# Kernel tuning notes

Hardware: AMD Instinct MI355X
Metric: run time of the kernel (lower is better)

Reference implementation:

```python
import jax, jax.numpy as jnp
import numpy as np

N = 8192  # num_nodes
E = 8192  # num_edges (== N so self-loops sit on the diagonal)
C = 256   # in_channels
ALPHA = 0.1
BETA = 0.5


def setup_inputs() -> dict:
    key = jax.random.key(0)
    k1, k2, k3 = jax.random.split(key, 3)
    x_0 = jax.random.normal(k1, (N, C), dtype=jnp.float32)
    # binary hypergraph incidence with self-loops on the diagonal
    mask = (jax.random.uniform(k2, (N, E)) < 0.004).astype(jnp.float32)
    idx = jnp.arange(N)
    incidence_1 = mask.at[idx, idx].set(1.0)
    # torch Linear(C, C, bias=False) weight, Kaiming-uniform-ish scale
    W = jax.random.normal(k3, (C, C), dtype=jnp.float32) / jnp.sqrt(C)
    return {"x_0": x_0, "incidence_1": incidence_1, "W": W}


def reference(x_0, incidence_1, W):
    # 1) edge aggregation: m_{0->1} = B^T x  -> [E, C]
    m_0_1 = incidence_1.T @ x_0
    # degree normalization (matches diag/to_dense math without materializing diag)
    node_degree = jnp.sum(incidence_1, axis=1)                      # [N]
    edge_degree = (node_degree @ incidence_1) / jnp.sum(incidence_1, axis=0)  # [E]
    # 2) node aggregation with 1/sqrt(d_z), 1/sqrt(d_x) scaling
    m_1_0 = (incidence_1 @ (m_0_1 / jnp.sqrt(edge_degree)[:, None])) \
            / jnp.sqrt(node_degree)[:, None]                        # [N, C]
    # 3) skip + learned update (x_skip defaults to x_0)
    x_combined = (1.0 - ALPHA) * m_1_0 + ALPHA * x_0
    return (1.0 - BETA) * x_combined + BETA * (x_combined @ W.T)
```

## Files before the change

### kernel.cpp

```cpp
#include <hip/hip_runtime.h>
#include <hip/hip_bf16.h>

#define NN 8192
#define NE 8192
#define CC 256
#define CAP 128

typedef __attribute__((ext_vector_type(8))) short bf16x8;
typedef __attribute__((ext_vector_type(8))) unsigned short u16x8;
typedef __attribute__((ext_vector_type(4))) float f32x4;

static __device__ __forceinline__ ushort f2b(float f) {
    unsigned u = __float_as_uint(f);
    return (ushort)((u + 0x7fffu + ((u >> 16) & 1u)) >> 16);
}
static __device__ __forceinline__ float b2f(ushort u) {
    return __uint_as_float((unsigned)u << 16);
}

__global__ __launch_bounds__(256) void k1_scan(const float* __restrict__ B,
                                               const float* __restrict__ x0,
                                               const float* __restrict__ W,
                                               ushort* __restrict__ x0b,
                                               ushort* __restrict__ Wb,
                                               int* __restrict__ csr,
                                               int* __restrict__ row_cnt,
                                               int* __restrict__ col_cnt,
                                               int* __restrict__ csc,
                                               float* __restrict__ edge_wsum) {
    {
        int i = blockIdx.x * 1024 + threadIdx.x * 4;
        float4 v = *(const float4*)(x0 + i);
        ushort4 u; u.x = f2b(v.x); u.y = f2b(v.y); u.z = f2b(v.z); u.w = f2b(v.w);
        *(ushort4*)(x0b + i) = u;
        if (blockIdx.x < 64) {
            float4 w = *(const float4*)(W + i);
            ushort4 uw; uw.x = f2b(w.x); uw.y = f2b(w.y); uw.z = f2b(w.z); uw.w = f2b(w.w);
            *(ushort4*)(Wb + i) = uw;
        }
    }
    const int wave = threadIdx.x >> 6;
    const int lane = threadIdx.x & 63;
    const int row  = blockIdx.x * 4 + wave;
    const float4* rp = (const float4*)(B + (size_t)row * NE);
    int* outp = csr + (size_t)row * CAP;
    const unsigned long long mlt = (1ull << lane) - 1ull;
    int base = 0;
    for (int it = 0; it < NE / 256; ++it) {
        float4 v = rp[it * 64 + lane];
        unsigned long long bx = __ballot(v.x != 0.f);
        unsigned long long by = __ballot(v.y != 0.f);
        unsigned long long bz = __ballot(v.z != 0.f);
        unsigned long long bw = __ballot(v.w != 0.f);
        if (!(bx | by | bz | bw)) continue;
        int tx = __popcll(bx), ty = __popcll(by), tz = __popcll(bz), tw = __popcll(bw);
        int e0 = (it * 64 + lane) * 4;
        int p;
        if (v.x != 0.f) { p = base + __popcll(bx & mlt);                if (p < CAP) outp[p] = e0;     }
        if (v.y != 0.f) { p = base + tx + __popcll(by & mlt);           if (p < CAP) outp[p] = e0 + 1; }
        if (v.z != 0.f) { p = base + tx + ty + __popcll(bz & mlt);      if (p < CAP) outp[p] = e0 + 2; }
        if (v.w != 0.f) { p = base + tx + ty + tz + __popcll(bw & mlt); if (p < CAP) outp[p] = e0 + 3; }
        base += tx + ty + tz + tw;
    }
    const int cnt = base < CAP ? base : CAP;
    if (lane == 0) row_cnt[row] = cnt;
    const float deg = (float)cnt;
    for (int i = lane; i < cnt; i += 64) {
        int e = outp[i];
        int pos = atomicAdd(&col_cnt[e], 1);
        if (pos < CAP) csc[(size_t)e * CAP + pos] = row;
        atomicAdd(&edge_wsum[e], deg);
    }
}

__global__ __launch_bounds__(256) void k4_edge_agg(const ushort* __restrict__ x0b,
                                                   const int* __restrict__ csc,
                                                   const int* __restrict__ col_cnt,
                                                   const float* __restrict__ edge_wsum,
                                                   ushort* __restrict__ m01s) {
    const int wave = threadIdx.x >> 6;
    const int lane = threadIdx.x & 63;
    const int half = lane >> 5;
    const int cl = lane & 31;
    const int e = blockIdx.x * 4 + wave;
    int cnt = col_cnt[e]; if (cnt > CAP) cnt = CAP;
    const float er = rsqrtf(edge_wsum[e] / (float)cnt);
    const int* cp = csc + (size_t)e * CAP;
    const int idx = cp[lane];
    const ushort* xb = x0b + cl * 8;
    float a0[8] = {}, a1[8] = {};
    const int lim = cnt < 64 ? cnt : 64;
    int i = 0;
    for (; i + 4 <= lim; i += 4) {
        int na = __shfl(idx, i + half);
        int nb = __shfl(idx, i + 2 + half);
        u16x8 a = *(const u16x8*)(xb + (size_t)na * CC);
        u16x8 b = *(const u16x8*)(xb + (size_t)nb * CC);
        #pragma unroll
        for (int c = 0; c < 8; ++c) { a0[c] += b2f(a[c]); a1[c] += b2f(b[c]); }
    }
    if (i + 2 <= lim) {
        int na = __shfl(idx, i + half);
        u16x8 a = *(const u16x8*)(xb + (size_t)na * CC);
        #pragma unroll
        for (int c = 0; c < 8; ++c) a0[c] += b2f(a[c]);
        i += 2;
    }
    if (i < lim) {
        int na = __shfl(idx, i);
        if (half == 0) {
            u16x8 a = *(const u16x8*)(xb + (size_t)na * CC);
            #pragma unroll
            for (int c = 0; c < 8; ++c) a0[c] += b2f(a[c]);
        }
    }
    if (cnt > 64 && half == 0) {
        for (int j = 64; j < cnt; ++j) {
            int n2 = cp[j];
            u16x8 a = *(const u16x8*)(xb + (size_t)n2 * CC);
            #pragma unroll
            for (int c = 0; c < 8; ++c) a0[c] += b2f(a[c]);
        }
    }
    u16x8 r8;
    #pragma unroll
    for (int c = 0; c < 8; ++c) {
        float t = a0[c] + a1[c];
        t += __shfl_xor(t, 32);
        r8[c] = f2b(t * er);
    }
    if (half == 0) *(u16x8*)(m01s + (size_t)e * CC + cl * 8) = r8;
}

__global__ __launch_bounds__(1024, 8) void k5_fused(const ushort* __restrict__ x0b,
                                                    const ushort* __restrict__ m01s,
                                                    const int* __restrict__ csr,
                                                    const int* __restrict__ row_cnt,
                                                    const ushort* __restrict__ Wb,
                                                    float* __restrict__ out) {
    __shared__ __align__(16) ushort xs[16][264];
    const int w = threadIdx.x >> 6;
    const int lane = threadIdx.x & 63;
    const int half = lane >> 5;
    const int cl = lane & 31;
    const int n = blockIdx.x * 16 + w;
    const int cnt = row_cnt[n];
    const float nr = rsqrtf((float)cnt);
    const int* ep = csr + (size_t)n * CAP;
    const int idx = ep[lane];
    const ushort* mb = m01s + cl * 8;
    float a0[8] = {}, a1[8] = {};
    const int lim = cnt < 64 ? cnt : 64;
    int i = 0;
    for (; i + 4 <= lim; i += 4) {
        int ea = __shfl(idx, i + half);
        int eb = __shfl(idx, i + 2 + half);
        u16x8 a = *(const u16x8*)(mb + (size_t)ea * CC);
        u16x8 b = *(const u16x8*)(mb + (size_t)eb * CC);
        #pragma unroll
        for (int c = 0; c < 8; ++c) { a0[c] += b2f(a[c]); a1[c] += b2f(b[c]); }
    }
    if (i + 2 <= lim) {
        int ea = __shfl(idx, i + half);
        u16x8 a = *(const u16x8*)(mb + (size_t)ea * CC);
        #pragma unroll
        for (int c = 0; c < 8; ++c) a0[c] += b2f(a[c]);
        i += 2;
    }
    if (i < lim) {
        int ea = __shfl(idx, i);
        if (half == 0) {
            u16x8 a = *(const u16x8*)(mb + (size_t)ea * CC);
            #pragma unroll
            for (int c = 0; c < 8; ++c) a0[c] += b2f(a[c]);
        }
    }
    if (cnt > 64 && half == 0) {
        for (int j = 64; j < cnt; ++j) {
            int e2 = ep[j];
            u16x8 a = *(const u16x8*)(mb + (size_t)e2 * CC);
            #pragma unroll
            for (int c = 0; c < 8; ++c) a0[c] += b2f(a[c]);
        }
    }
    u16x8 x = *(const u16x8*)(x0b + (size_t)n * CC + cl * 8);
    const float s = 0.9f * nr;
    u16x8 r8;
    #pragma unroll
    for (int c = 0; c < 8; ++c) {
        float t = a0[c] + a1[c];
        t += __shfl_xor(t, 32);
        r8[c] = f2b(s * t + 0.1f * b2f(x[c]));
    }
    if (half == 0) *(u16x8*)(&xs[w][cl * 8]) = r8;
    __syncthreads();
    const int lr = lane & 15, lk = lane >> 4;
    const int n0 = w * 16;
    f32x4 acc = {0.f, 0.f, 0.f, 0.f};
    #pragma unroll
    for (int kb = 0; kb < 8; ++kb) {
        bf16x8 a = *(const bf16x8*)(&xs[lr][kb * 32 + lk * 8]);
        bf16x8 b = *(const bf16x8*)(Wb + (size_t)(n0 + lr) * CC + kb * 32 + lk * 8);
        acc = __builtin_amdgcn_mfma_f32_16x16x32_bf16(a, b, acc, 0, 0, 0);
    }
    const size_t rb = (size_t)blockIdx.x * 16;
    #pragma unroll
    for (int r = 0; r < 4; ++r) {
        int row = lk * 4 + r;
        int col = n0 + lr;
        float sk = b2f(xs[row][col]);
        out[(rb + row) * CC + col] = 0.5f * sk + 0.5f * acc[r];
    }
}

extern "C" void kernel_launch(void* const* d_in, const int* in_sizes, int n_in,
                              void* d_out, int out_size, void* d_ws, size_t ws_size,
                              hipStream_t stream) {
    const float* x0 = (const float*)d_in[0];
    const float* B  = (const float*)d_in[1];
    const float* W  = (const float*)d_in[2];
    float* out = (float*)d_out;

    char* ws = (char*)d_ws;
    const size_t need = (17ull << 20) + 4ull * NE * 4;
    if (ws_size < need) return;

    int*    csr       = (int*)(ws);
    int*    csc       = (int*)(ws + (4ull << 20));
    ushort* m01s      = (ushort*)(ws + (8ull << 20));
    ushort* x0b       = (ushort*)(ws + (12ull << 20));
    ushort* Wb        = (ushort*)(ws + (16ull << 20));
    int*    row_cnt   = (int*)(ws + (16ull << 20) + (256u << 10));
    int*    col_cnt   = row_cnt + NN;
    float*  edge_wsum = (float*)(col_cnt + NE);

    hipMemsetAsync(col_cnt, 0, 2ull * NE * 4, stream);

    k1_scan<<<NN / 4, 256, 0, stream>>>(B, x0, W, x0b, Wb, csr, row_cnt, col_cnt, csc, edge_wsum);
    k4_edge_agg<<<NE / 4, 256, 0, stream>>>(x0b, csc, col_cnt, edge_wsum, m01s);
    k5_fused<<<NN / 16, 1024, 0, stream>>>(x0b, m01s, csr, row_cnt, Wb, out);
}
```

Before: 104.7 us.

## Prefetch incidence rows in scan and deepen gather unrolling in aggregation kernels

The incidence-row scan now loads the next float4 before processing the current one. It replaces the four-ballot prefix compaction with a per-wave LDS atomic counter that hands each lane a slot range sized by the sum of its four values. The edge and node aggregation kernels now keep four gathered rows in flight per iteration instead of two, to raise memory-level parallelism. The LDS atomic makes the order of CSR entries nondeterministic. Using the value sum as the nonzero count assumes the incidence is strictly binary.

Measured after the change: 103.8 us. Within noise of the previous version (-0.8%).

```diff
diff --git a/kernel.cpp b/kernel.cpp
--- a/kernel.cpp
+++ b/kernel.cpp
@@ -28,6 +28,7 @@
                                                int* __restrict__ col_cnt,
                                                int* __restrict__ csc,
                                                float* __restrict__ edge_wsum) {
+    __shared__ int wcnt[4];
     {
         int i = blockIdx.x * 1024 + threadIdx.x * 4;
         float4 v = *(const float4*)(x0 + i);
@@ -44,25 +45,27 @@
     const int row  = blockIdx.x * 4 + wave;
     const float4* rp = (const float4*)(B + (size_t)row * NE);
     int* outp = csr + (size_t)row * CAP;
-    const unsigned long long mlt = (1ull << lane) - 1ull;
-    int base = 0;
-    for (int it = 0; it < NE / 256; ++it) {
-        float4 v = rp[it * 64 + lane];
-        unsigned long long bx = __ballot(v.x != 0.f);
-        unsigned long long by = __ballot(v.y != 0.f);
-        unsigned long long bz = __ballot(v.z != 0.f);
-        unsigned long long bw = __ballot(v.w != 0.f);
-        if (!(bx | by | bz | bw)) continue;
-        int tx = __popcll(bx), ty = __popcll(by), tz = __popcll(bz), tw = __popcll(bw);
-        int e0 = (it * 64 + lane) * 4;
-        int p;
-        if (v.x != 0.f) { p = base + __popcll(bx & mlt);                if (p < CAP) outp[p] = e0;     }
-        if (v.y != 0.f) { p = base + tx + __popcll(by & mlt);           if (p < CAP) outp[p] = e0 + 1; }
-        if (v.z != 0.f) { p = base + tx + ty + __popcll(bz & mlt);      if (p < CAP) outp[p] = e0 + 2; }
-        if (v.w != 0.f) { p = base + tx + ty + tz + __popcll(bw & mlt); if (p < CAP) outp[p] = e0 + 3; }
-        base += tx + ty + tz + tw;
-    }
-    const int cnt = base < CAP ? base : CAP;
+    if (lane == 0) wcnt[wave] = 0;
+    float4 v = rp[lane];
+    #pragma unroll 1
+    for (int it = 0; it < 32; ++it) {
+        float4 vn = v;
+        if (it < 31) vn = rp[(it + 1) * 64 + lane];
+        float fs = v.x + v.y + v.z + v.w;
+        if (__ballot(fs != 0.f)) {
+            int m = (int)fs;
+            int pos = 0;
+            if (m) pos = atomicAdd(&wcnt[wave], m);
+            int e0 = (it * 64 + lane) * 4;
+            if (v.x != 0.f) { if (pos < CAP) outp[pos] = e0;     ++pos; }
+            if (v.y != 0.f) { if (pos < CAP) outp[pos] = e0 + 1; ++pos; }
+            if (v.z != 0.f) { if (pos < CAP) outp[pos] = e0 + 2; ++pos; }
+            if (v.w != 0.f) { if (pos < CAP) outp[pos] = e0 + 3; ++pos; }
+        }
+        v = vn;
+    }
+    int cnt = wcnt[wave];
+    cnt = cnt < CAP ? cnt : CAP;
     if (lane == 0) row_cnt[row] = cnt;
     const float deg = (float)cnt;
     for (int i = lane; i < cnt; i += 64) {
@@ -91,35 +94,41 @@
     float a0[8] = {}, a1[8] = {};
     const int lim = cnt < 64 ? cnt : 64;
     int i = 0;
-    for (; i + 4 <= lim; i += 4) {
-        int na = __shfl(idx, i + half);
-        int nb = __shfl(idx, i + 2 + half);
-        u16x8 a = *(const u16x8*)(xb + (size_t)na * CC);
-        u16x8 b = *(const u16x8*)(xb + (size_t)nb * CC);
-        #pragma unroll
-        for (int c = 0; c < 8; ++c) { a0[c] += b2f(a[c]); a1[c] += b2f(b[c]); }
-    }
-    if (i + 2 <= lim) {
-        int na = __shfl(idx, i + half);
-        u16x8 a = *(const u16x8*)(xb + (size_t)na * CC);
-        #pragma unroll
-        for (int c = 0; c < 8; ++c) a0[c] += b2f(a[c]);
-        i += 2;
+    for (; i + 8 <= lim; i += 8) {
+        int n0 = __shfl(idx, i + half);
+        int n1 = __shfl(idx, i + 2 + half);
+        int n2 = __shfl(idx, i + 4 + half);
+        int n3 = __shfl(idx, i + 6 + half);
+        u16x8 r0 = *(const u16x8*)(xb + (size_t)n0 * CC);
+        u16x8 r1 = *(const u16x8*)(xb + (size_t)n1 * CC);
+        u16x8 r2 = *(const u16x8*)(xb + (size_t)n2 * CC);
+        u16x8 r3 = *(const u16x8*)(xb + (size_t)n3 * CC);
+        #pragma unroll
+        for (int c = 0; c < 8; ++c) {
+            a0[c] += b2f(r0[c]); a1[c] += b2f(r1[c]);
+            a0[c] += b2f(r2[c]); a1[c] += b2f(r3[c]);
+        }
+    }
+    for (; i + 2 <= lim; i += 2) {
+        int n0 = __shfl(idx, i + half);
+        u16x8 r0 = *(const u16x8*)(xb + (size_t)n0 * CC);
+        #pragma unroll
+        for (int c = 0; c < 8; ++c) a0[c] += b2f(r0[c]);
     }
     if (i < lim) {
-        int na = __shfl(idx, i);
+        int n0 = __shfl(idx, i);
         if (half == 0) {
-            u16x8 a = *(const u16x8*)(xb + (size_t)na * CC);
-            #pragma unroll
-            for (int c = 0; c < 8; ++c) a0[c] += b2f(a[c]);
+            u16x8 r0 = *(const u16x8*)(xb + (size_t)n0 * CC);
+            #pragma unroll
+            for (int c = 0; c < 8; ++c) a0[c] += b2f(r0[c]);
         }
     }
     if (cnt > 64 && half == 0) {
         for (int j = 64; j < cnt; ++j) {
             int n2 = cp[j];
-            u16x8 a = *(const u16x8*)(xb + (size_t)n2 * CC);
-            #pragma unroll
-            for (int c = 0; c < 8; ++c) a0[c] += b2f(a[c]);
+            u16x8 r0 = *(const u16x8*)(xb + (size_t)n2 * CC);
+            #pragma unroll
+            for (int c = 0; c < 8; ++c) a0[c] += b2f(r0[c]);
         }
     }
     u16x8 r8;
@@ -152,35 +161,41 @@
     float a0[8] = {}, a1[8] = {};
     const int lim = cnt < 64 ? cnt : 64;
     int i = 0;
-    for (; i + 4 <= lim; i += 4) {
-        int ea = __shfl(idx, i + half);
-        int eb = __shfl(idx, i + 2 + half);
-        u16x8 a = *(const u16x8*)(mb + (size_t)ea * CC);
-        u16x8 b = *(const u16x8*)(mb + (size_t)eb * CC);
-        #pragma unroll
-        for (int c = 0; c < 8; ++c) { a0[c] += b2f(a[c]); a1[c] += b2f(b[c]); }
-    }
-    if (i + 2 <= lim) {
-        int ea = __shfl(idx, i + half);
-        u16x8 a = *(const u16x8*)(mb + (size_t)ea * CC);
-        #pragma unroll
-        for (int c = 0; c < 8; ++c) a0[c] += b2f(a[c]);
-        i += 2;
+    for (; i + 8 <= lim; i += 8) {
+        int e0 = __shfl(idx, i + half);
+        int e1 = __shfl(idx, i + 2 + half);
+        int e2 = __shfl(idx, i + 4 + half);
+        int e3 = __shfl(idx, i + 6 + half);
+        u16x8 r0 = *(const u16x8*)(mb + (size_t)e0 * CC);
+        u16x8 r1 = *(const u16x8*)(mb + (size_t)e1 * CC);
+        u16x8 r2 = *(const u16x8*)(mb + (size_t)e2 * CC);
+        u16x8 r3 = *(const u16x8*)(mb + (size_t)e3 * CC);
+        #pragma unroll
+        for (int c = 0; c < 8; ++c) {
+            a0[c] += b2f(r0[c]); a1[c] += b2f(r1[c]);
+            a0[c] += b2f(r2[c]); a1[c] += b2f(r3[c]);
+        }
+    }
+    for (; i + 2 <= lim; i += 2) {
+        int e0 = __shfl(idx, i + half);
+        u16x8 r0 = *(const u16x8*)(mb + (size_t)e0 * CC);
+        #pragma unroll
+        for (int c = 0; c < 8; ++c) a0[c] += b2f(r0[c]);
     }
     if (i < lim) {
-        int ea = __shfl(idx, i);
+        int e0 = __shfl(idx, i);
         if (half == 0) {
-            u16x8 a = *(const u16x8*)(mb + (size_t)ea * CC);
-            #pragma unroll
-            for (int c = 0; c < 8; ++c) a0[c] += b2f(a[c]);
+            u16x8 r0 = *(const u16x8*)(mb + (size_t)e0 * CC);
+            #pragma unroll
+            for (int c = 0; c < 8; ++c) a0[c] += b2f(r0[c]);
         }
     }
     if (cnt > 64 && half == 0) {
         for (int j = 64; j < cnt; ++j) {
             int e2 = ep[j];
-            u16x8 a = *(const u16x8*)(mb + (size_t)e2 * CC);
-            #pragma unroll
-            for (int c = 0; c < 8; ++c) a0[c] += b2f(a[c]);
+            u16x8 r0 = *(const u16x8*)(mb + (size_t)e2 * CC);
+            #pragma unroll
+            for (int c = 0; c < 8; ++c) a0[c] += b2f(r0[c]);
         }
     }
     u16x8 x = *(const u16x8*)(x0b + (size_t)n * CC + cl * 8);
```

## Scan incidence by column panels and fuse edge aggregation into scan kernel

Applied to the files above, without the earlier changes.

Replaces the row-wise scan plus separate edge-aggregation kernel with a column-panel scan that builds CSC lists in shared memory and immediately gathers x0 rows for each edge. Edge-degree normalisation moves out of the edge pass into a small kernel and is applied per edge inside the node aggregation instead. CSR is built with global atomics per row, so neighbour order in each row is no longer deterministic, and x0 conversion moves to a separate kernel. The aim is to drop the memset and global CSC atomics, at the cost of one more launch and strided column-panel reads of the dense incidence matrix.

Result: slower. 147.3 us (+40.7%).

```diff
diff --git a/kernel.cpp b/kernel.cpp
--- a/kernel.cpp
+++ b/kernel.cpp
@@ -5,6 +5,7 @@
 #define NE 8192
 #define CC 256
 #define CAP 128
+#define PNL 32
 
 typedef __attribute__((ext_vector_type(8))) short bf16x8;
 typedef __attribute__((ext_vector_type(8))) unsigned short u16x8;
@@ -18,124 +19,137 @@
     return __uint_as_float((unsigned)u << 16);
 }
 
-__global__ __launch_bounds__(256) void k1_scan(const float* __restrict__ B,
-                                               const float* __restrict__ x0,
-                                               const float* __restrict__ W,
-                                               ushort* __restrict__ x0b,
-                                               ushort* __restrict__ Wb,
-                                               int* __restrict__ csr,
-                                               int* __restrict__ row_cnt,
-                                               int* __restrict__ col_cnt,
-                                               int* __restrict__ csc,
-                                               float* __restrict__ edge_wsum) {
-    {
-        int i = blockIdx.x * 1024 + threadIdx.x * 4;
-        float4 v = *(const float4*)(x0 + i);
-        ushort4 u; u.x = f2b(v.x); u.y = f2b(v.y); u.z = f2b(v.z); u.w = f2b(v.w);
-        *(ushort4*)(x0b + i) = u;
-        if (blockIdx.x < 64) {
-            float4 w = *(const float4*)(W + i);
-            ushort4 uw; uw.x = f2b(w.x); uw.y = f2b(w.y); uw.z = f2b(w.z); uw.w = f2b(w.w);
-            *(ushort4*)(Wb + i) = uw;
-        }
-    }
-    const int wave = threadIdx.x >> 6;
-    const int lane = threadIdx.x & 63;
-    const int row  = blockIdx.x * 4 + wave;
-    const float4* rp = (const float4*)(B + (size_t)row * NE);
-    int* outp = csr + (size_t)row * CAP;
-    const unsigned long long mlt = (1ull << lane) - 1ull;
-    int base = 0;
-    for (int it = 0; it < NE / 256; ++it) {
-        float4 v = rp[it * 64 + lane];
-        unsigned long long bx = __ballot(v.x != 0.f);
-        unsigned long long by = __ballot(v.y != 0.f);
-        unsigned long long bz = __ballot(v.z != 0.f);
-        unsigned long long bw = __ballot(v.w != 0.f);
-        if (!(bx | by | bz | bw)) continue;
-        int tx = __popcll(bx), ty = __popcll(by), tz = __popcll(bz), tw = __popcll(bw);
-        int e0 = (it * 64 + lane) * 4;
-        int p;
-        if (v.x != 0.f) { p = base + __popcll(bx & mlt);                if (p < CAP) outp[p] = e0;     }
-        if (v.y != 0.f) { p = base + tx + __popcll(by & mlt);           if (p < CAP) outp[p] = e0 + 1; }
-        if (v.z != 0.f) { p = base + tx + ty + __popcll(bz & mlt);      if (p < CAP) outp[p] = e0 + 2; }
-        if (v.w != 0.f) { p = base + tx + ty + tz + __popcll(bw & mlt); if (p < CAP) outp[p] = e0 + 3; }
-        base += tx + ty + tz + tw;
-    }
-    const int cnt = base < CAP ? base : CAP;
-    if (lane == 0) row_cnt[row] = cnt;
-    const float deg = (float)cnt;
-    for (int i = lane; i < cnt; i += 64) {
-        int e = outp[i];
-        int pos = atomicAdd(&col_cnt[e], 1);
-        if (pos < CAP) csc[(size_t)e * CAP + pos] = row;
-        atomicAdd(&edge_wsum[e], deg);
-    }
-}
-
-__global__ __launch_bounds__(256) void k4_edge_agg(const ushort* __restrict__ x0b,
-                                                   const int* __restrict__ csc,
-                                                   const int* __restrict__ col_cnt,
-                                                   const float* __restrict__ edge_wsum,
-                                                   ushort* __restrict__ m01s) {
-    const int wave = threadIdx.x >> 6;
-    const int lane = threadIdx.x & 63;
-    const int half = lane >> 5;
-    const int cl = lane & 31;
+__global__ __launch_bounds__(256) void k0_convert(const float* __restrict__ x0,
+                                                  const float* __restrict__ W,
+                                                  ushort* __restrict__ x0b,
+                                                  ushort* __restrict__ Wb,
+                                                  int* __restrict__ row_cnt) {
+    const int t = blockIdx.x * 256 + threadIdx.x;
+    const int i = t * 8;
+    f32x4 v0 = *(const f32x4*)(x0 + i);
+    f32x4 v1 = *(const f32x4*)(x0 + i + 4);
+    u16x8 u;
+    u[0]=f2b(v0.x); u[1]=f2b(v0.y); u[2]=f2b(v0.z); u[3]=f2b(v0.w);
+    u[4]=f2b(v1.x); u[5]=f2b(v1.y); u[6]=f2b(v1.z); u[7]=f2b(v1.w);
+    *(u16x8*)(x0b + i) = u;
+    if (i < CC * CC) {
+        f32x4 w0 = *(const f32x4*)(W + i);
+        f32x4 w1 = *(const f32x4*)(W + i + 4);
+        u16x8 uw;
+        uw[0]=f2b(w0.x); uw[1]=f2b(w0.y); uw[2]=f2b(w0.z); uw[3]=f2b(w0.w);
+        uw[4]=f2b(w1.x); uw[5]=f2b(w1.y); uw[6]=f2b(w1.z); uw[7]=f2b(w1.w);
+        *(u16x8*)(Wb + i) = uw;
+    }
+    if (t < NN) row_cnt[t] = 0;
+}
+
+__global__ __launch_bounds__(1024) void k1_panel(const float* __restrict__ B,
+                                                 const ushort* __restrict__ x0b,
+                                                 int* __restrict__ csr,
+                                                 int* __restrict__ row_cnt,
+                                                 int* __restrict__ col_cnt,
+                                                 int* __restrict__ csc,
+                                                 ushort* __restrict__ m01s) {
+    __shared__ int ecnt[PNL];
+    __shared__ int cloc[PNL][CAP];
+    const int tid = threadIdx.x, w = tid >> 6, lane = tid & 63;
+    const int e0 = blockIdx.x * PNL;
+    if (tid < PNL) ecnt[tid] = 0;
+    __syncthreads();
+    const int lr = lane >> 3;
+    const int lc = (lane & 7) * 4;
+    const float* Bp = B + e0 + lc;
+    const int rbase = w * 8 + lr;
+    f32x4 buf[4];
+    #pragma unroll
+    for (int p = 0; p < 4; ++p)
+        buf[p] = *(const f32x4*)(Bp + (size_t)(p * 128 + rbase) * NE);
+    #pragma unroll 1
+    for (int it = 0; it < 64; ++it) {
+        f32x4 v = buf[it & 3];
+        if (it + 4 < 64)
+            buf[it & 3] = *(const f32x4*)(Bp + (size_t)((it + 4) * 128 + rbase) * NE);
+        float fs = v.x + v.y + v.z + v.w;
+        if (__ballot(fs != 0.f)) {
+            if (fs != 0.f) {
+                const int row = it * 128 + rbase;
+                int p0 = atomicAdd(&row_cnt[row], (int)fs);
+                if (v.x != 0.f) { if (p0 < CAP) csr[(size_t)row*CAP+p0] = e0+lc;   ++p0;
+                                  int q = atomicAdd(&ecnt[lc],   1); if (q < CAP) cloc[lc][q]   = row; }
+                if (v.y != 0.f) { if (p0 < CAP) csr[(size_t)row*CAP+p0] = e0+lc+1; ++p0;
+                                  int q = atomicAdd(&ecnt[lc+1], 1); if (q < CAP) cloc[lc+1][q] = row; }
+                if (v.z != 0.f) { if (p0 < CAP) csr[(size_t)row*CAP+p0] = e0+lc+2; ++p0;
+                                  int q = atomicAdd(&ecnt[lc+2], 1); if (q < CAP) cloc[lc+2][q] = row; }
+                if (v.w != 0.f) { if (p0 < CAP) csr[(size_t)row*CAP+p0] = e0+lc+3; ++p0;
+                                  int q = atomicAdd(&ecnt[lc+3], 1); if (q < CAP) cloc[lc+3][q] = row; }
+            }
+        }
+    }
+    __syncthreads();
+    for (int e = w; e < PNL; e += 16) {
+        int cnt = ecnt[e]; if (cnt > CAP) cnt = CAP;
+        if (lane == 0) col_cnt[e0 + e] = cnt;
+        for (int i = lane; i < cnt; i += 64) csc[(size_t)(e0 + e) * CAP + i] = cloc[e][i];
+    }
+    const int half = lane >> 5, cl = lane & 31;
+    const ushort* xb = x0b + cl * 8;
+    #pragma unroll 1
+    for (int ee = w * 2; ee < w * 2 + 2; ++ee) {
+        int cnt = ecnt[ee]; if (cnt > CAP) cnt = CAP;
+        float a0[8] = {}, a1[8] = {};
+        int i = 0;
+        for (; i + 4 <= cnt; i += 4) {
+            int na = cloc[ee][i + half];
+            int nb = cloc[ee][i + 2 + half];
+            u16x8 ra = *(const u16x8*)(xb + (size_t)na * CC);
+            u16x8 rb = *(const u16x8*)(xb + (size_t)nb * CC);
+            #pragma unroll
+            for (int c = 0; c < 8; ++c) { a0[c] += b2f(ra[c]); a1[c] += b2f(rb[c]); }
+        }
+        if (i + 2 <= cnt) {
+            int na = cloc[ee][i + half];
+            u16x8 ra = *(const u16x8*)(xb + (size_t)na * CC);
+            #pragma unroll
+            for (int c = 0; c < 8; ++c) a0[c] += b2f(ra[c]);
+            i += 2;
+        }
+        if (i < cnt && half == 0) {
+            int na = cloc[ee][i];
+            u16x8 ra = *(const u16x8*)(xb + (size_t)na * CC);
+            #pragma unroll
+            for (int c = 0; c < 8; ++c) a0[c] += b2f(ra[c]);
+        }
+        u16x8 r8;
+        #pragma unroll
+        for (int c = 0; c < 8; ++c) {
+            float t = a0[c] + a1[c];
+            t += __shfl_xor(t, 32);
+            r8[c] = f2b(t);
+        }
+        if (half == 0) *(u16x8*)(m01s + (size_t)(e0 + ee) * CC + cl * 8) = r8;
+    }
+}
+
+__global__ __launch_bounds__(256) void k2_er(const int* __restrict__ csc,
+                                             const int* __restrict__ col_cnt,
+                                             const int* __restrict__ row_cnt,
+                                             float* __restrict__ er) {
+    const int wave = threadIdx.x >> 6, lane = threadIdx.x & 63;
     const int e = blockIdx.x * 4 + wave;
     int cnt = col_cnt[e]; if (cnt > CAP) cnt = CAP;
-    const float er = rsqrtf(edge_wsum[e] / (float)cnt);
-    const int* cp = csc + (size_t)e * CAP;
-    const int idx = cp[lane];
-    const ushort* xb = x0b + cl * 8;
-    float a0[8] = {}, a1[8] = {};
-    const int lim = cnt < 64 ? cnt : 64;
-    int i = 0;
-    for (; i + 4 <= lim; i += 4) {
-        int na = __shfl(idx, i + half);
-        int nb = __shfl(idx, i + 2 + half);
-        u16x8 a = *(const u16x8*)(xb + (size_t)na * CC);
-        u16x8 b = *(const u16x8*)(xb + (size_t)nb * CC);
-        #pragma unroll
-        for (int c = 0; c < 8; ++c) { a0[c] += b2f(a[c]); a1[c] += b2f(b[c]); }
-    }
-    if (i + 2 <= lim) {
-        int na = __shfl(idx, i + half);
-        u16x8 a = *(const u16x8*)(xb + (size_t)na * CC);
-        #pragma unroll
-        for (int c = 0; c < 8; ++c) a0[c] += b2f(a[c]);
-        i += 2;
-    }
-    if (i < lim) {
-        int na = __shfl(idx, i);
-        if (half == 0) {
-            u16x8 a = *(const u16x8*)(xb + (size_t)na * CC);
-            #pragma unroll
-            for (int c = 0; c < 8; ++c) a0[c] += b2f(a[c]);
-        }
-    }
-    if (cnt > 64 && half == 0) {
-        for (int j = 64; j < cnt; ++j) {
-            int n2 = cp[j];
-            u16x8 a = *(const u16x8*)(xb + (size_t)n2 * CC);
-            #pragma unroll
-            for (int c = 0; c < 8; ++c) a0[c] += b2f(a[c]);
-        }
-    }
-    u16x8 r8;
-    #pragma unroll
-    for (int c = 0; c < 8; ++c) {
-        float t = a0[c] + a1[c];
-        t += __shfl_xor(t, 32);
-        r8[c] = f2b(t * er);
-    }
-    if (half == 0) *(u16x8*)(m01s + (size_t)e * CC + cl * 8) = r8;
+    float s = 0.f;
+    for (int i = lane; i < cnt; i += 64)
+        s += (float)row_cnt[csc[(size_t)e * CAP + i]];
+    #pragma unroll
+    for (int d = 1; d < 64; d <<= 1) s += __shfl_xor(s, d);
+    if (lane == 0) er[e] = rsqrtf(s / (float)cnt);
 }
 
 __global__ __launch_bounds__(1024, 8) void k5_fused(const ushort* __restrict__ x0b,
                                                     const ushort* __restrict__ m01s,
                                                     const int* __restrict__ csr,
                                                     const int* __restrict__ row_cnt,
+                                                    const float* __restrict__ er,
                                                     const ushort* __restrict__ Wb,
                                                     float* __restrict__ out) {
     __shared__ __align__(16) ushort xs[16][264];
@@ -144,43 +158,54 @@
     const int half = lane >> 5;
     const int cl = lane & 31;
     const int n = blockIdx.x * 16 + w;
-    const int cnt = row_cnt[n];
-    const float nr = rsqrtf((float)cnt);
+    const int cnt_true = row_cnt[n];
+    const int cnt = cnt_true < CAP ? cnt_true : CAP;
+    const float nr = rsqrtf((float)cnt_true);
     const int* ep = csr + (size_t)n * CAP;
     const int idx = ep[lane];
     const ushort* mb = m01s + cl * 8;
     float a0[8] = {}, a1[8] = {};
     const int lim = cnt < 64 ? cnt : 64;
     int i = 0;
-    for (; i + 4 <= lim; i += 4) {
-        int ea = __shfl(idx, i + half);
-        int eb = __shfl(idx, i + 2 + half);
-        u16x8 a = *(const u16x8*)(mb + (size_t)ea * CC);
-        u16x8 b = *(const u16x8*)(mb + (size_t)eb * CC);
+    for (; i + 8 <= lim; i += 8) {
+        int f0 = __shfl(idx, i + half);
+        int f1 = __shfl(idx, i + 2 + half);
+        int f2 = __shfl(idx, i + 4 + half);
+        int f3 = __shfl(idx, i + 6 + half);
+        float w0 = er[f0], w1 = er[f1], w2 = er[f2], w3 = er[f3];
+        u16x8 r0 = *(const u16x8*)(mb + (size_t)f0 * CC);
+        u16x8 r1 = *(const u16x8*)(mb + (size_t)f1 * CC);
+        u16x8 r2 = *(const u16x8*)(mb + (size_t)f2 * CC);
+        u16x8 r3 = *(const u16x8*)(mb + (size_t)f3 * CC);
         #pragma unroll
-        for (int c = 0; c < 8; ++c) { a0[c] += b2f(a[c]); a1[c] += b2f(b[c]); }
-    }
-    if (i + 2 <= lim) {
-        int ea = __shfl(idx, i + half);
-        u16x8 a = *(const u16x8*)(mb + (size_t)ea * CC);
+        for (int c = 0; c < 8; ++c) {
+            a0[c] += w0 * b2f(r0[c]); a1[c] += w1 * b2f(r1[c]);
+            a0[c] += w2 * b2f(r2[c]); a1[c] += w3 * b2f(r3[c]);
+        }
+    }
+    for (; i + 2 <= lim; i += 2) {
+        int f0 = __shfl(idx, i + half);
+        float w0 = er[f0];
+        u16x8 r0 = *(const u16x8*)(mb + (size_t)f0 * CC);
         #pragma unroll
-        for (int c = 0; c < 8; ++c) a0[c] += b2f(a[c]);
-        i += 2;
+        for (int c = 0; c < 8; ++c) a0[c] += w0 * b2f(r0[c]);
     }
     if (i < lim) {
-        int ea = __shfl(idx, i);
+        int f0 = __shfl(idx, i);
         if (half == 0) {
-            u16x8 a = *(const u16x8*)(mb + (size_t)ea * CC);
-            #pragma unroll
-            for (int c = 0; c < 8; ++c) a0[c] += b2f(a[c]);
+            float w0 = er[f0];
+            u16x8 r0 = *(const u16x8*)(mb + (size_t)f0 * CC);
+            #pragma unroll
+            for (int c = 0; c < 8; ++c) a0[c] += w0 * b2f(r0[c]);
         }
     }
     if (cnt > 64 && half == 0) {
         for (int j = 64; j < cnt; ++j) {
-            int e2 = ep[j];
-            u16x8 a = *(const u16x8*)(mb + (size_t)e2 * CC);
-            #pragma unroll
-            for (int c = 0; c < 8; ++c) a0[c] += b2f(a[c]);
+            int f0 = ep[j];
+            float w0 = er[f0];
+            u16x8 r0 = *(const u16x8*)(mb + (size_t)f0 * CC);
+            #pragma unroll
+            for (int c = 0; c < 8; ++c) a0[c] += w0 * b2f(r0[c]);
         }
     }
     u16x8 x = *(const u16x8*)(x0b + (size_t)n * CC + cl * 8);
@@ -222,21 +247,20 @@
     float* out = (float*)d_out;
 
     char* ws = (char*)d_ws;
-    const size_t need = (17ull << 20) + 4ull * NE * 4;
+    const size_t need = (16ull << 20) + (512ull << 10);
     if (ws_size < need) return;
 
-    int*    csr       = (int*)(ws);
-    int*    csc       = (int*)(ws + (4ull << 20));
-    ushort* m01s      = (ushort*)(ws + (8ull << 20));
-    ushort* x0b       = (ushort*)(ws + (12ull << 20));
-    ushort* Wb        = (ushort*)(ws + (16ull << 20));
-    int*    row_cnt   = (int*)(ws + (16ull << 20) + (256u << 10));
-    int*    col_cnt   = row_cnt + NN;
-    float*  edge_wsum = (float*)(col_cnt + NE);
-
-    hipMemsetAsync(col_cnt, 0, 2ull * NE * 4, stream);
-
-    k1_scan<<<NN / 4, 256, 0, stream>>>(B, x0, W, x0b, Wb, csr, row_cnt, col_cnt, csc, edge_wsum);
-    k4_edge_agg<<<NE / 4, 256, 0, stream>>>(x0b, csc, col_cnt, edge_wsum, m01s);
-    k5_fused<<<NN / 16, 1024, 0, stream>>>(x0b, m01s, csr, row_cnt, Wb, out);
-}
+    int*    csr     = (int*)(ws);
+    int*    csc     = (int*)(ws + (4ull << 20));
+    ushort* m01s    = (ushort*)(ws + (8ull << 20));
+    ushort* x0b     = (ushort*)(ws + (12ull << 20));
+    ushort* Wb      = (ushort*)(ws + (16ull << 20));
+    int*    row_cnt = (int*)(ws + (16ull << 20) + (256u << 10));
+    int*    col_cnt = row_cnt + NN;
+    float*  er      = (float*)(col_cnt + NE);
+
+    k0_convert<<<NN * CC / 8 / 256, 256, 0, stream>>>(x0, W, x0b, Wb, row_cnt);
+    k1_panel<<<NE / PNL, 1024, 0, stream>>>(B, x0b, csr, row_cnt, col_cnt, csc, m01s);
+    k2_er<<<NE / 4, 256, 0, stream>>>(csc, col_cnt, row_cnt, er);
+    k5_fused<<<NN / 16, 1024, 0, stream>>>(x0b, m01s, csr, row_cnt, er, Wb, out);
+}
```
